# Kernel tuning notes

Measured on AMD Instinct MI355X. Metric: run time of the kernel, lower is better.

The kernel has to match this reference:

```python
import jax, jax.numpy as jnp
import numpy as np

S, B, E, H, V = 512, 128, 1024, 1024, 50257

def setup_inputs() -> dict:
    key = jax.random.key(0)
    ks = jax.random.split(key, 6)
    scale = 1.0 / np.sqrt(H)
    return {
        "X": jax.random.randint(ks[0], (S, B), 0, V),
        "embd_weight": jax.random.normal(ks[1], (V, E), dtype=jnp.float32),
        "W_ih": jax.random.uniform(ks[2], (4 * H, E), minval=-scale, maxval=scale, dtype=jnp.float32),
        "W_hh": jax.random.uniform(ks[3], (4 * H, H), minval=-scale, maxval=scale, dtype=jnp.float32),
        "b_ih": jax.random.uniform(ks[4], (4 * H,), minval=-scale, maxval=scale, dtype=jnp.float32),
        "b_hh": jax.random.uniform(ks[5], (4 * H,), minval=-scale, maxval=scale, dtype=jnp.float32),
    }

def reference(X, embd_weight, W_ih, W_hh, b_ih, b_hh):
    # X: [S, B] int indices -> embedded [S, B, E]
    emb = embd_weight[X]
    b = b_ih + b_hh  # [4H]
    Bsz = X.shape[1]
    h0 = jnp.zeros((Bsz, H), dtype=emb.dtype)
    c0 = jnp.zeros((Bsz, H), dtype=emb.dtype)

    def step(carry, xt):
        h, c = carry
        # PyTorch LSTM gate order: i, f, g, o
        gates = xt @ W_ih.T + h @ W_hh.T + b  # [B, 4H]
        i, f, g, o = jnp.split(gates, 4, axis=-1)
        c_new = jax.nn.sigmoid(f) * c + jax.nn.sigmoid(i) * jnp.tanh(g)
        h_new = jax.nn.sigmoid(o) * jnp.tanh(c_new)
        return (h_new, c_new), None

    (h_last, _), _ = jax.lax.scan(step, (h0, c0), emb)
    yt = h_last[None]  # [1, B, H] — output of last timestep
    # Faithful to source: LogSoftmax(dim=1) normalizes over the BATCH axis
    return jax.nn.log_softmax(yt, axis=1)
```

## Files before the change

### kernel.cpp

```cpp
#include <hip/hip_runtime.h>
#include <cstdint>
#include <cstddef>

#define SEQ   512
#define BATCH 128
#define EMB   1024
#define HID   1024
#define VOCAB 50257
#define GATES 4096

typedef _Float16 f16x8 __attribute__((ext_vector_type(8)));
typedef float    f32x4 __attribute__((ext_vector_type(4)));
typedef unsigned short u16;
typedef u16 u16x8 __attribute__((ext_vector_type(8)));

__device__ inline u16 f2h(float x) { union { _Float16 h; u16 u; } c; c.h = (_Float16)x; return c.u; }
__device__ inline float h2f(u16 u) { union { u16 u; _Float16 h; } c; c.u = u; return (float)c.h; }

__global__ void cast_f32_f16_kernel(const float* __restrict__ src, u16* __restrict__ dst, int n4) {
  int i = blockIdx.x * blockDim.x + threadIdx.x;
  int stride = gridDim.x * blockDim.x;
  for (; i < n4; i += stride) {
    float4 v = ((const float4*)src)[i];
    ushort4 o;
    o.x = f2h(v.x); o.y = f2h(v.y); o.z = f2h(v.z); o.w = f2h(v.w);
    ((ushort4*)dst)[i] = o;
  }
}

__global__ void init_kernel(const float* __restrict__ bih, const float* __restrict__ bhh,
                            float* __restrict__ bias, u16* __restrict__ h0, int* __restrict__ sync) {
  int i = blockIdx.x * blockDim.x + threadIdx.x;
  if (i < GATES) bias[i] = bih[i] + bhh[i];
  ushort4 z; z.x = z.y = z.z = z.w = 0;
  ((ushort4*)h0)[i] = z;
  if (i < 8192) sync[i] = 0;
}

__global__ __launch_bounds__(256) void embed_gemm(
    const u16* __restrict__ embw, const u16* __restrict__ wih,
    const int* __restrict__ X, u16* __restrict__ gx, int t0)
{
  __shared__ u16 Als[4096];
  __shared__ u16 Bls[4096];
  const int tid = threadIdx.x;
  const int w = tid >> 6, lane = tid & 63;
  const int T = t0 + blockIdx.y;
  const int colbase = blockIdx.x << 7;
  const int wm = w & 1, wn = w >> 1;
  f32x4 acc[4][4] = {};
  const u16* afp = Als + (lane >> 4) * 1024 + (wm * 64 + (lane & 15)) * 8;
  const u16* bfp = Bls + (lane >> 4) * 1024 + (wn * 64 + (lane & 15)) * 8;

  int skq[4], srow[4], shalf[4];
  size_t sg[4];
#pragma unroll
  for (int s = 0; s < 4; ++s) {
    const int idx = s * 256 + tid;
    shalf[s] = idx >> 9; skq[s] = (idx >> 7) & 3; srow[s] = idx & 127;
    if (shalf[s] == 0) sg[s] = (size_t)X[(size_t)T * BATCH + srow[s]] * EMB + skq[s] * 8;
    else               sg[s] = (size_t)(colbase + srow[s]) * EMB + skq[s] * 8;
  }

  for (int kit = 0; kit < 32; ++kit) {
    u16x8 v[4];
#pragma unroll
    for (int s = 0; s < 4; ++s)
      v[s] = *(const u16x8*)((shalf[s] ? wih : embw) + sg[s] + kit * 32);
#pragma unroll
    for (int s = 0; s < 4; ++s)
      *(u16x8*)((shalf[s] ? Bls : Als) + skq[s] * 1024 + srow[s] * 8) = v[s];
    __syncthreads();
    f16x8 af[4], bf[4];
#pragma unroll
    for (int mt = 0; mt < 4; ++mt) af[mt] = *(const f16x8*)(afp + mt * 128);
#pragma unroll
    for (int nt = 0; nt < 4; ++nt) bf[nt] = *(const f16x8*)(bfp + nt * 128);
#pragma unroll
    for (int mt = 0; mt < 4; ++mt)
#pragma unroll
      for (int nt = 0; nt < 4; ++nt)
        acc[mt][nt] = __builtin_amdgcn_mfma_f32_16x16x32_f16(af[mt], bf[nt], acc[mt][nt], 0, 0, 0);
    __syncthreads();
  }
  const size_t outbase = (size_t)blockIdx.y * ((size_t)GATES * BATCH);
#pragma unroll
  for (int mt = 0; mt < 4; ++mt) {
#pragma unroll
    for (int nt = 0; nt < 4; ++nt) {
      const int n  = colbase + wn * 64 + nt * 16 + (lane & 15);
      const int b0 = wm * 64 + mt * 16 + ((lane >> 4) << 2);
#pragma unroll
      for (int p = 0; p < 4; ++p)
        gx[outbase + (size_t)(b0 + p) * GATES + n] = f2h(acc[mt][nt][p]);
    }
  }
}

__global__ __launch_bounds__(256, 1) void lstm_kernel(
    const u16* __restrict__ whh, const float* __restrict__ bias,
    const u16* __restrict__ gx, u16* __restrict__ hring,
    float* __restrict__ cstate, float* __restrict__ hlast,
    int* __restrict__ flags, int t0, int t1)
{
  extern __shared__ u16 LdsRaw[];
  f32x4* Red = (f32x4*)LdsRaw;
  const int tid = threadIdx.x;
  const int w = tid >> 6, lane = tid & 63;
  const int jloc = lane & 15, lq = lane >> 4;
  const int bh = blockIdx.x & 1;
  const int jw = blockIdx.x >> 1;

  f16x8 wreg[4][8];
#pragma unroll
  for (int g = 0; g < 4; ++g)
#pragma unroll
    for (int ks = 0; ks < 8; ++ks)
      wreg[g][ks] = *(const f16x8*)(whh + ((size_t)g * HID + jw * 16 + jloc) * HID
                                          + w * 256 + ks * 32 + lq * 8);

  const int b  = bh * 64 + w * 16 + jloc;
  const int j0 = jw * 16 + lq * 4;
  f32x4 bs[4];
#pragma unroll
  for (int g = 0; g < 4; ++g) bs[g] = *(const f32x4*)(bias + g * HID + j0);

  f32x4 cc;
  if (t0 == 0) { cc[0] = cc[1] = cc[2] = cc[3] = 0.f; }
  else cc = *(const f32x4*)(cstate + (size_t)b * HID + j0);

  const u16* hb = hring + (size_t)(w * 32 + lq) * 1024 + (size_t)(bh * 64 + jloc) * 8;
  const int hw_idx = (jw * 2 + (lq >> 1)) * 1024 + b * 8 + (lq & 1) * 4;
  const u16* gbase = gx + (size_t)b * GATES + j0;
  const int* fpoll = flags + ((w * 16 + (lane & 15)) * 2 + bh) * 32;

  ushort4 vX[4];
#pragma unroll
  for (int g = 0; g < 4; ++g) vX[g] = *(const ushort4*)(gbase + g * 1024);

  for (int t = t0; t < t1; ++t) {
    if (t > t0) {
      for (;;) {
        int a = __hip_atomic_load(fpoll, __ATOMIC_RELAXED, __HIP_MEMORY_SCOPE_AGENT);
        if (__all(a >= t)) break;
        __builtin_amdgcn_s_sleep(1);
      }
      asm volatile("" ::: "memory");
      __builtin_amdgcn_sched_barrier(0);
    }
    const u16* ap = hb + (size_t)t * (BATCH * HID);
    f16x8 av[8][4];
#pragma unroll
    for (int ks = 0; ks < 8; ++ks)
#pragma unroll
      for (int nt = 0; nt < 4; ++nt)
        av[ks][nt] = *(const f16x8*)(ap + ks * 4096 + nt * 128);
    __builtin_amdgcn_sched_barrier(0);
    f32x4 acc[4][4] = {};
#pragma unroll
    for (int ks = 0; ks < 8; ++ks)
#pragma unroll
      for (int g = 0; g < 4; ++g)
#pragma unroll
        for (int nt = 0; nt < 4; ++nt)
          acc[g][nt] = __builtin_amdgcn_mfma_f32_16x16x32_f16(wreg[g][ks], av[ks][nt], acc[g][nt], 0, 0, 0);
#pragma unroll
    for (int g = 0; g < 4; ++g)
#pragma unroll
      for (int nt = 0; nt < 4; ++nt)
        if (nt != w) Red[((w * 4 + g) * 4 + nt) * 64 + lane] = acc[g][nt];
    __syncthreads();
    f32x4 gate[4];
#pragma unroll
    for (int g = 0; g < 4; ++g) {
      gate[g] = acc[g][w];
#pragma unroll
      for (int wp = 0; wp < 4; ++wp)
        if (wp != w) gate[g] += Red[((wp * 4 + g) * 4 + w) * 64 + lane];
    }
    u16* hout = hring + (size_t)(t + 1) * (BATCH * HID);
    float hn4[4];
#pragma unroll
    for (int p = 0; p < 4; ++p) {
      float gi = gate[0][p] + h2f(((const u16*)&vX[0])[p]) + bs[0][p];
      float gf = gate[1][p] + h2f(((const u16*)&vX[1])[p]) + bs[1][p];
      float gg = gate[2][p] + h2f(((const u16*)&vX[2])[p]) + bs[2][p];
      float go = gate[3][p] + h2f(((const u16*)&vX[3])[p]) + bs[3][p];
      float ii = 1.f / (1.f + __expf(-gi));
      float ff = 1.f / (1.f + __expf(-gf));
      float e2 = __expf(-2.f * fabsf(gg));
      float tg = copysignf((1.f - e2) / (1.f + e2), gg);
      float oo = 1.f / (1.f + __expf(-go));
      float cn = ff * cc[p] + ii * tg;
      cc[p] = cn;
      float e2c = __expf(-2.f * fabsf(cn));
      float tc = copysignf((1.f - e2c) / (1.f + e2c), cn);
      hn4[p] = oo * tc;
    }
    unsigned long long hp = (unsigned long long)f2h(hn4[0])
                          | ((unsigned long long)f2h(hn4[1]) << 16)
                          | ((unsigned long long)f2h(hn4[2]) << 32)
                          | ((unsigned long long)f2h(hn4[3]) << 48);
    __hip_atomic_store((unsigned long long*)(hout + hw_idx), hp,
                       __ATOMIC_RELAXED, __HIP_MEMORY_SCOPE_AGENT);
    if (t + 1 == SEQ) {
      float4 hl; hl.x = hn4[0]; hl.y = hn4[1]; hl.z = hn4[2]; hl.w = hn4[3];
      *(float4*)(hlast + (size_t)b * HID + j0) = hl;
    }
    asm volatile("s_waitcnt vmcnt(0)" ::: "memory");
    __builtin_amdgcn_sched_barrier(0);
    __builtin_amdgcn_s_barrier();
    if (t + 1 < t1) {
      if (tid == 0)
        __hip_atomic_store(flags + blockIdx.x * 32, t + 1,
                           __ATOMIC_RELAXED, __HIP_MEMORY_SCOPE_AGENT);
      const size_t off = (size_t)(t + 1 - t0) * ((size_t)GATES * BATCH);
#pragma unroll
      for (int g = 0; g < 4; ++g) vX[g] = *(const ushort4*)(gbase + off + g * 1024);
    }
  }
  *(f32x4*)(cstate + (size_t)b * HID + j0) = cc;
}

__global__ void logsoftmax_kernel(const float* __restrict__ hlast, float* __restrict__ out) {
  const int j = blockIdx.x * blockDim.x + threadIdx.x;
  if (j >= HID) return;
  float m = -1e30f;
  for (int b = 0; b < BATCH; ++b) m = fmaxf(m, hlast[(size_t)b * HID + j]);
  float s = 0.f;
  for (int b = 0; b < BATCH; ++b) s += expf(hlast[(size_t)b * HID + j] - m);
  const float lse = m + logf(s);
  for (int b = 0; b < BATCH; ++b) out[(size_t)b * HID + j] = hlast[(size_t)b * HID + j] - lse;
}

extern "C" void kernel_launch(void* const* d_in, const int* in_sizes, int n_in,
                              void* d_out, int out_size, void* d_ws, size_t ws_size,
                              hipStream_t stream) {
  const int*   X    = (const int*)d_in[0];
  const float* embd = (const float*)d_in[1];
  const float* wih  = (const float*)d_in[2];
  const float* whh  = (const float*)d_in[3];
  const float* bih  = (const float*)d_in[4];
  const float* bhh  = (const float*)d_in[5];
  float* out = (float*)d_out;

  char* p = (char*)d_ws;
  auto alloc = [&](size_t bytes) { char* r = p; p += (bytes + 255) & ~(size_t)255; return r; };
  u16*   embw    = (u16*)alloc((size_t)VOCAB * EMB * 2);
  u16*   wihh    = (u16*)alloc((size_t)GATES * EMB * 2);
  u16*   whhh    = (u16*)alloc((size_t)GATES * HID * 2);
  float* bias    = (float*)alloc((size_t)GATES * 4);
  u16*   hring   = (u16*)alloc((size_t)(SEQ + 1) * BATCH * HID * 2);
  float* hlast   = (float*)alloc((size_t)BATCH * HID * 4);
  float* cst     = (float*)alloc((size_t)BATCH * HID * 4);
  int*   flags   = (int*)alloc(32768);
  size_t used = (size_t)(p - (char*)d_ws);
  size_t avail = ws_size > used ? ws_size - used : 0;
  long long Tc = (long long)(avail / ((size_t)GATES * BATCH * 2));
  if (Tc > SEQ) Tc = SEQ;
  if (Tc < 1) return;
  u16* gx = (u16*)alloc((size_t)Tc * GATES * BATCH * 2);

  hipFuncSetAttribute((const void*)lstm_kernel, hipFuncAttributeMaxDynamicSharedMemorySize, 65536);

  cast_f32_f16_kernel<<<2048, 256, 0, stream>>>(embd, embw, VOCAB * EMB / 4);
  cast_f32_f16_kernel<<<256, 256, 0, stream>>>(wih, wihh, GATES * EMB / 4);
  cast_f32_f16_kernel<<<256, 256, 0, stream>>>(whh, whhh, GATES * HID / 4);
  init_kernel<<<128, 256, 0, stream>>>(bih, bhh, bias, hring, flags);
  for (int t0 = 0; t0 < SEQ; t0 += (int)Tc) {
    const int t1 = (t0 + (int)Tc < SEQ) ? t0 + (int)Tc : SEQ;
    dim3 grid(32, t1 - t0);
    embed_gemm<<<grid, 256, 0, stream>>>(embw, wihh, X, gx, t0);
    lstm_kernel<<<128, 256, 65536, stream>>>(whhh, bias, gx, hring, cst, hlast, flags, t0, t1);
  }
  logsoftmax_kernel<<<4, 256, 0, stream>>>(hlast, out);
}
```

Baseline: 4.804 ms.

## Fuse embedding GEMM, LSTM recurrence and log-softmax into one persistent producer-consumer kernel

Replaces the separate embed_gemm, lstm_kernel and logsoftmax launches with a single persistent kernel of 256 blocks. Blocks 128-255 compute the input-projection tiles into a ring buffer and publish per-timestep counters, while blocks 0-127 run the recurrence and wait on those counters, so the input GEMM overlaps the serial LSTM steps. The GEMM loop also gains a four-deep register prefetch of global loads. This relies on all 256 blocks being co-resident and adds spin-wait traffic, with a risk of deadlock if residency is not guaranteed.

Result: faster. 4.012 ms (-16.5%).

```diff
diff --git a/kernel.cpp b/kernel.cpp
--- a/kernel.cpp
+++ b/kernel.cpp
@@ -37,76 +37,104 @@
   if (i < 8192) sync[i] = 0;
 }
 
-__global__ __launch_bounds__(256) void embed_gemm(
+__global__ __launch_bounds__(256, 1) void fused_kernel(
     const u16* __restrict__ embw, const u16* __restrict__ wih,
-    const int* __restrict__ X, u16* __restrict__ gx, int t0)
+    const u16* __restrict__ whh, const float* __restrict__ bias,
+    const int* __restrict__ X, u16* __restrict__ gx,
+    u16* __restrict__ hring, float* __restrict__ hlast,
+    float* __restrict__ out, int* __restrict__ flags, int Tc)
 {
-  __shared__ u16 Als[4096];
-  __shared__ u16 Bls[4096];
+  extern __shared__ u16 LdsRaw[];
   const int tid = threadIdx.x;
   const int w = tid >> 6, lane = tid & 63;
-  const int T = t0 + blockIdx.y;
-  const int colbase = blockIdx.x << 7;
-  const int wm = w & 1, wn = w >> 1;
-  f32x4 acc[4][4] = {};
-  const u16* afp = Als + (lane >> 4) * 1024 + (wm * 64 + (lane & 15)) * 8;
-  const u16* bfp = Bls + (lane >> 4) * 1024 + (wn * 64 + (lane & 15)) * 8;
-
-  int skq[4], srow[4], shalf[4];
-  size_t sg[4];
-#pragma unroll
-  for (int s = 0; s < 4; ++s) {
-    const int idx = s * 256 + tid;
-    shalf[s] = idx >> 9; skq[s] = (idx >> 7) & 3; srow[s] = idx & 127;
-    if (shalf[s] == 0) sg[s] = (size_t)X[(size_t)T * BATCH + srow[s]] * EMB + skq[s] * 8;
-    else               sg[s] = (size_t)(colbase + srow[s]) * EMB + skq[s] * 8;
-  }
-
-  for (int kit = 0; kit < 32; ++kit) {
-    u16x8 v[4];
-#pragma unroll
-    for (int s = 0; s < 4; ++s)
-      v[s] = *(const u16x8*)((shalf[s] ? wih : embw) + sg[s] + kit * 32);
-#pragma unroll
-    for (int s = 0; s < 4; ++s)
-      *(u16x8*)((shalf[s] ? Bls : Als) + skq[s] * 1024 + srow[s] * 8) = v[s];
-    __syncthreads();
-    f16x8 af[4], bf[4];
-#pragma unroll
-    for (int mt = 0; mt < 4; ++mt) af[mt] = *(const f16x8*)(afp + mt * 128);
-#pragma unroll
-    for (int nt = 0; nt < 4; ++nt) bf[nt] = *(const f16x8*)(bfp + nt * 128);
-#pragma unroll
-    for (int mt = 0; mt < 4; ++mt)
-#pragma unroll
-      for (int nt = 0; nt < 4; ++nt)
-        acc[mt][nt] = __builtin_amdgcn_mfma_f32_16x16x32_f16(af[mt], bf[nt], acc[mt][nt], 0, 0, 0);
-    __syncthreads();
-  }
-  const size_t outbase = (size_t)blockIdx.y * ((size_t)GATES * BATCH);
-#pragma unroll
-  for (int mt = 0; mt < 4; ++mt) {
-#pragma unroll
-    for (int nt = 0; nt < 4; ++nt) {
-      const int n  = colbase + wn * 64 + nt * 16 + (lane & 15);
-      const int b0 = wm * 64 + mt * 16 + ((lane >> 4) << 2);
-#pragma unroll
-      for (int p = 0; p < 4; ++p)
-        gx[outbase + (size_t)(b0 + p) * GATES + n] = f2h(acc[mt][nt][p]);
-    }
-  }
-}
-
-__global__ __launch_bounds__(256, 1) void lstm_kernel(
-    const u16* __restrict__ whh, const float* __restrict__ bias,
-    const u16* __restrict__ gx, u16* __restrict__ hring,
-    float* __restrict__ cstate, float* __restrict__ hlast,
-    int* __restrict__ flags, int t0, int t1)
-{
-  extern __shared__ u16 LdsRaw[];
+  int* gxcnt = flags + 4096;
+
+  if (blockIdx.x >= 128) {
+    u16* Als = LdsRaw;
+    u16* Bls = LdsRaw + 4096;
+    const int ewg = blockIdx.x - 128;
+    const int wm = w & 1, wn = w >> 1;
+    const u16* afp = Als + (lane >> 4) * 1024 + (wm * 64 + (lane & 15)) * 8;
+    const u16* bfp = Bls + (lane >> 4) * 1024 + (wn * 64 + (lane & 15)) * 8;
+    int skq[4], srow[4], shalf[4];
+#pragma unroll
+    for (int s = 0; s < 4; ++s) {
+      const int idx = s * 256 + tid;
+      shalf[s] = idx >> 9; skq[s] = (idx >> 7) & 3; srow[s] = idx & 127;
+    }
+    for (int tile = ewg; tile < SEQ * 32; tile += 128) {
+      const int T = tile >> 5;
+      const int colbase = (tile & 31) << 7;
+      if (T >= Tc) {
+        const int need = T - Tc + 1;
+        for (;;) {
+          int f = __hip_atomic_load(flags + (tid & 127) * 32,
+                                    __ATOMIC_RELAXED, __HIP_MEMORY_SCOPE_AGENT);
+          if (__syncthreads_and(f >= need)) break;
+          __builtin_amdgcn_s_sleep(8);
+        }
+      }
+      size_t sg[4];
+#pragma unroll
+      for (int s = 0; s < 4; ++s) {
+        if (shalf[s] == 0) sg[s] = (size_t)X[(size_t)T * BATCH + srow[s]] * EMB + skq[s] * 8;
+        else               sg[s] = (size_t)(colbase + srow[s]) * EMB + skq[s] * 8;
+      }
+      f32x4 acc[4][4] = {};
+      u16x8 vq[4][4];
+#pragma unroll
+      for (int d = 0; d < 4; ++d)
+#pragma unroll
+        for (int s = 0; s < 4; ++s)
+          vq[d][s] = *(const u16x8*)((shalf[s] ? wih : embw) + sg[s] + d * 32);
+      for (int kb = 0; kb < 32; kb += 4) {
+#pragma unroll
+        for (int d = 0; d < 4; ++d) {
+#pragma unroll
+          for (int s = 0; s < 4; ++s)
+            *(u16x8*)((shalf[s] ? Bls : Als) + skq[s] * 1024 + srow[s] * 8) = vq[d][s];
+          __syncthreads();
+          if (kb + d + 4 < 32) {
+#pragma unroll
+            for (int s = 0; s < 4; ++s)
+              vq[d][s] = *(const u16x8*)((shalf[s] ? wih : embw) + sg[s] + (kb + d + 4) * 32);
+          }
+          f16x8 af[4], bf[4];
+#pragma unroll
+          for (int mt = 0; mt < 4; ++mt) af[mt] = *(const f16x8*)(afp + mt * 128);
+#pragma unroll
+          for (int nt = 0; nt < 4; ++nt) bf[nt] = *(const f16x8*)(bfp + nt * 128);
+#pragma unroll
+          for (int mt = 0; mt < 4; ++mt)
+#pragma unroll
+            for (int nt = 0; nt < 4; ++nt)
+              acc[mt][nt] = __builtin_amdgcn_mfma_f32_16x16x32_f16(af[mt], bf[nt], acc[mt][nt], 0, 0, 0);
+          __syncthreads();
+        }
+      }
+      const size_t outbase = (size_t)(T % Tc) * ((size_t)GATES * BATCH);
+#pragma unroll
+      for (int mt = 0; mt < 4; ++mt) {
+#pragma unroll
+        for (int nt = 0; nt < 4; ++nt) {
+          const int n  = colbase + wn * 64 + nt * 16 + (lane & 15);
+          const int b0 = wm * 64 + mt * 16 + ((lane >> 4) << 2);
+#pragma unroll
+          for (int p = 0; p < 4; ++p)
+            __hip_atomic_store(gx + outbase + (size_t)(b0 + p) * GATES + n,
+                               f2h(acc[mt][nt][p]),
+                               __ATOMIC_RELAXED, __HIP_MEMORY_SCOPE_AGENT);
+        }
+      }
+      asm volatile("s_waitcnt vmcnt(0)" ::: "memory");
+      __syncthreads();
+      if (tid == 0)
+        __hip_atomic_fetch_add(gxcnt + T, 1, __ATOMIC_RELAXED, __HIP_MEMORY_SCOPE_AGENT);
+    }
+    return;
+  }
+
   f32x4* Red = (f32x4*)LdsRaw;
-  const int tid = threadIdx.x;
-  const int w = tid >> 6, lane = tid & 63;
   const int jloc = lane & 15, lq = lane >> 4;
   const int bh = blockIdx.x & 1;
   const int jw = blockIdx.x >> 1;
@@ -125,21 +153,31 @@
 #pragma unroll
   for (int g = 0; g < 4; ++g) bs[g] = *(const f32x4*)(bias + g * HID + j0);
 
-  f32x4 cc;
-  if (t0 == 0) { cc[0] = cc[1] = cc[2] = cc[3] = 0.f; }
-  else cc = *(const f32x4*)(cstate + (size_t)b * HID + j0);
+  f32x4 cc; cc[0] = cc[1] = cc[2] = cc[3] = 0.f;
 
   const u16* hb = hring + (size_t)(w * 32 + lq) * 1024 + (size_t)(bh * 64 + jloc) * 8;
   const int hw_idx = (jw * 2 + (lq >> 1)) * 1024 + b * 8 + (lq & 1) * 4;
   const u16* gbase = gx + (size_t)b * GATES + j0;
   const int* fpoll = flags + ((w * 16 + (lane & 15)) * 2 + bh) * 32;
 
-  ushort4 vX[4];
-#pragma unroll
-  for (int g = 0; g < 4; ++g) vX[g] = *(const ushort4*)(gbase + g * 1024);
-
-  for (int t = t0; t < t1; ++t) {
-    if (t > t0) {
+  int slot = 0;
+  unsigned long long vXu[4];
+  {
+    const int* cnt = gxcnt;
+    for (;;) {
+      int c = __hip_atomic_load(cnt, __ATOMIC_RELAXED, __HIP_MEMORY_SCOPE_AGENT);
+      if (c >= 32) break;
+      __builtin_amdgcn_s_sleep(1);
+    }
+    asm volatile("" ::: "memory");
+#pragma unroll
+    for (int g = 0; g < 4; ++g)
+      vXu[g] = __hip_atomic_load((const unsigned long long*)(gbase + g * 1024),
+                                 __ATOMIC_RELAXED, __HIP_MEMORY_SCOPE_AGENT);
+  }
+
+  for (int t = 0; t < SEQ; ++t) {
+    if (t > 0) {
       for (;;) {
         int a = __hip_atomic_load(fpoll, __ATOMIC_RELAXED, __HIP_MEMORY_SCOPE_AGENT);
         if (__all(a >= t)) break;
@@ -182,10 +220,10 @@
     float hn4[4];
 #pragma unroll
     for (int p = 0; p < 4; ++p) {
-      float gi = gate[0][p] + h2f(((const u16*)&vX[0])[p]) + bs[0][p];
-      float gf = gate[1][p] + h2f(((const u16*)&vX[1])[p]) + bs[1][p];
-      float gg = gate[2][p] + h2f(((const u16*)&vX[2])[p]) + bs[2][p];
-      float go = gate[3][p] + h2f(((const u16*)&vX[3])[p]) + bs[3][p];
+      float gi = gate[0][p] + h2f((u16)(vXu[0] >> (16 * p))) + bs[0][p];
+      float gf = gate[1][p] + h2f((u16)(vXu[1] >> (16 * p))) + bs[1][p];
+      float gg = gate[2][p] + h2f((u16)(vXu[2] >> (16 * p))) + bs[2][p];
+      float go = gate[3][p] + h2f((u16)(vXu[3] >> (16 * p))) + bs[3][p];
       float ii = 1.f / (1.f + __expf(-gi));
       float ff = 1.f / (1.f + __expf(-gf));
       float e2 = __expf(-2.f * fabsf(gg));
@@ -204,33 +242,54 @@
     __hip_atomic_store((unsigned long long*)(hout + hw_idx), hp,
                        __ATOMIC_RELAXED, __HIP_MEMORY_SCOPE_AGENT);
     if (t + 1 == SEQ) {
-      float4 hl; hl.x = hn4[0]; hl.y = hn4[1]; hl.z = hn4[2]; hl.w = hn4[3];
-      *(float4*)(hlast + (size_t)b * HID + j0) = hl;
+      union { float f[2]; unsigned long long u; } pk;
+      pk.f[0] = hn4[0]; pk.f[1] = hn4[1];
+      __hip_atomic_store((unsigned long long*)(hlast + (size_t)b * HID + j0), pk.u,
+                         __ATOMIC_RELAXED, __HIP_MEMORY_SCOPE_AGENT);
+      pk.f[0] = hn4[2]; pk.f[1] = hn4[3];
+      __hip_atomic_store((unsigned long long*)(hlast + (size_t)b * HID + j0 + 2), pk.u,
+                         __ATOMIC_RELAXED, __HIP_MEMORY_SCOPE_AGENT);
     }
     asm volatile("s_waitcnt vmcnt(0)" ::: "memory");
     __builtin_amdgcn_sched_barrier(0);
     __builtin_amdgcn_s_barrier();
-    if (t + 1 < t1) {
-      if (tid == 0)
-        __hip_atomic_store(flags + blockIdx.x * 32, t + 1,
-                           __ATOMIC_RELAXED, __HIP_MEMORY_SCOPE_AGENT);
-      const size_t off = (size_t)(t + 1 - t0) * ((size_t)GATES * BATCH);
-#pragma unroll
-      for (int g = 0; g < 4; ++g) vX[g] = *(const ushort4*)(gbase + off + g * 1024);
-    }
-  }
-  *(f32x4*)(cstate + (size_t)b * HID + j0) = cc;
-}
-
-__global__ void logsoftmax_kernel(const float* __restrict__ hlast, float* __restrict__ out) {
-  const int j = blockIdx.x * blockDim.x + threadIdx.x;
-  if (j >= HID) return;
-  float m = -1e30f;
-  for (int b = 0; b < BATCH; ++b) m = fmaxf(m, hlast[(size_t)b * HID + j]);
-  float s = 0.f;
-  for (int b = 0; b < BATCH; ++b) s += expf(hlast[(size_t)b * HID + j] - m);
-  const float lse = m + logf(s);
-  for (int b = 0; b < BATCH; ++b) out[(size_t)b * HID + j] = hlast[(size_t)b * HID + j] - lse;
+    if (tid == 0)
+      __hip_atomic_store(flags + blockIdx.x * 32, t + 1,
+                         __ATOMIC_RELAXED, __HIP_MEMORY_SCOPE_AGENT);
+    if (t + 1 < SEQ) {
+      slot = (slot + 1 == Tc) ? 0 : slot + 1;
+      const int* cnt = gxcnt + (t + 1);
+      for (;;) {
+        int c = __hip_atomic_load(cnt, __ATOMIC_RELAXED, __HIP_MEMORY_SCOPE_AGENT);
+        if (c >= 32) break;
+        __builtin_amdgcn_s_sleep(1);
+      }
+      asm volatile("" ::: "memory");
+      __builtin_amdgcn_sched_barrier(0);
+      const u16* gslot = gbase + (size_t)slot * ((size_t)GATES * BATCH);
+#pragma unroll
+      for (int g = 0; g < 4; ++g)
+        vXu[g] = __hip_atomic_load((const unsigned long long*)(gslot + g * 1024),
+                                   __ATOMIC_RELAXED, __HIP_MEMORY_SCOPE_AGENT);
+    }
+  }
+
+  if (blockIdx.x < 4) {
+    for (;;) {
+      int f = __hip_atomic_load(flags + (tid & 127) * 32,
+                                __ATOMIC_RELAXED, __HIP_MEMORY_SCOPE_AGENT);
+      if (__syncthreads_and(f >= SEQ)) break;
+      __builtin_amdgcn_s_sleep(4);
+    }
+    const int j = blockIdx.x * 256 + tid;
+    float m = -1e30f;
+    for (int b2 = 0; b2 < BATCH; ++b2) m = fmaxf(m, hlast[(size_t)b2 * HID + j]);
+    float s = 0.f;
+    for (int b2 = 0; b2 < BATCH; ++b2) s += expf(hlast[(size_t)b2 * HID + j] - m);
+    const float lse = m + logf(s);
+    for (int b2 = 0; b2 < BATCH; ++b2)
+      out[(size_t)b2 * HID + j] = hlast[(size_t)b2 * HID + j] - lse;
+  }
 }
 
 extern "C" void kernel_launch(void* const* d_in, const int* in_sizes, int n_in,
@@ -252,7 +311,6 @@
   float* bias    = (float*)alloc((size_t)GATES * 4);
   u16*   hring   = (u16*)alloc((size_t)(SEQ + 1) * BATCH * HID * 2);
   float* hlast   = (float*)alloc((size_t)BATCH * HID * 4);
-  float* cst     = (float*)alloc((size_t)BATCH * HID * 4);
   int*   flags   = (int*)alloc(32768);
   size_t used = (size_t)(p - (char*)d_ws);
   size_t avail = ws_size > used ? ws_size - used : 0;
@@ -260,18 +318,15 @@
   if (Tc > SEQ) Tc = SEQ;
   if (Tc < 1) return;
   u16* gx = (u16*)alloc((size_t)Tc * GATES * BATCH * 2);
-
-  hipFuncSetAttribute((const void*)lstm_kernel, hipFuncAttributeMaxDynamicSharedMemorySize, 65536);
+  int Tci = (int)Tc;
+
+  hipFuncSetAttribute((const void*)fused_kernel, hipFuncAttributeMaxDynamicSharedMemorySize, 98304);
 
   cast_f32_f16_kernel<<<2048, 256, 0, stream>>>(embd, embw, VOCAB * EMB / 4);
   cast_f32_f16_kernel<<<256, 256, 0, stream>>>(wih, wihh, GATES * EMB / 4);
   cast_f32_f16_kernel<<<256, 256, 0, stream>>>(whh, whhh, GATES * HID / 4);
   init_kernel<<<128, 256, 0, stream>>>(bih, bhh, bias, hring, flags);
-  for (int t0 = 0; t0 < SEQ; t0 += (int)Tc) {
-    const int t1 = (t0 + (int)Tc < SEQ) ? t0 + (int)Tc : SEQ;
-    dim3 grid(32, t1 - t0);
-    embed_gemm<<<grid, 256, 0, stream>>>(embw, wihh, X, gx, t0);
-    lstm_kernel<<<128, 256, 65536, stream>>>(whhh, bias, gx, hring, cst, hlast, flags, t0, t1);
-  }
-  logsoftmax_kernel<<<4, 256, 0, stream>>>(hlast, out);
+
+  fused_kernel<<<dim3(256), dim3(256), 98304, stream>>>(
+      embw, wihh, whhh, bias, X, gx, hring, hlast, out, flags, Tci);
 }
```
